# Kernel tuning notes

Measured on AMD Instinct MI355X. Metric: run time of the kernel, lower is better.

## Reference

```python
import jax, jax.numpy as jnp
import numpy as np

N = 100000
E = 1600000
IN_FEATS = 128
N_HIDDEN = 128
N_CLASSES = 40
EPS = 1e-5


def _gconv(x, W, b, src, dst, n):
    # DGL GraphConv with norm='both': D_out^{-1/2} A D_in^{-1/2} X W (+ b), degrees clamped to >=1
    ones = jnp.ones(src.shape[0], x.dtype)
    out_deg = jnp.clip(jax.ops.segment_sum(ones, src, num_segments=n), 1.0)
    in_deg = jnp.clip(jax.ops.segment_sum(ones, dst, num_segments=n), 1.0)
    h = x * (out_deg ** -0.5)[:, None]
    agg = jax.ops.segment_sum(h[src], dst, num_segments=n)  # SpMM
    agg = agg * (in_deg ** -0.5)[:, None]
    out = agg @ W
    return out + b if b is not None else out


def setup_inputs() -> dict:
    key = jax.random.key(0)
    ks = jax.random.split(key, 16)
    s = lambda fan: 1.0 / np.sqrt(fan)
    feat = jax.random.normal(ks[0], (N, IN_FEATS), dtype=jnp.float32)
    src = jax.random.randint(ks[1], (E,), 0, N, dtype=jnp.int32)
    dst = jax.random.randint(ks[2], (E,), 0, N, dtype=jnp.int32)
    # backward convs: in_feats -> in_hidden (128->128 all layers); bias only at last layer
    Wb = jax.random.uniform(ks[3], (3, IN_FEATS, N_HIDDEN), jnp.float32, -s(IN_FEATS), s(IN_FEATS))
    bb2 = jax.random.uniform(ks[4], (N_HIDDEN,), jnp.float32, -s(IN_FEATS), s(IN_FEATS))
    # forward convs: layers 0,1 are 128->128, layer 2 is 128->40 with bias
    Wh01 = jax.random.uniform(ks[5], (2, N_HIDDEN, N_HIDDEN), jnp.float32, -s(N_HIDDEN), s(N_HIDDEN))
    W2 = jax.random.uniform(ks[6], (N_HIDDEN, N_CLASSES), jnp.float32, -s(N_HIDDEN), s(N_HIDDEN))
    b2 = jax.random.uniform(ks[7], (N_CLASSES,), jnp.float32, -s(N_HIDDEN), s(N_HIDDEN))
    # linear branch (use_linear=True), no bias
    Wl01 = jax.random.uniform(ks[8], (2, N_HIDDEN, N_HIDDEN), jnp.float32, -s(N_HIDDEN), s(N_HIDDEN))
    Wl2 = jax.random.uniform(ks[9], (N_HIDDEN, N_CLASSES), jnp.float32, -s(N_HIDDEN), s(N_HIDDEN))
    gamma = jnp.ones((2, N_HIDDEN), jnp.float32)
    beta = jnp.zeros((2, N_HIDDEN), jnp.float32)
    return {"feat": feat, "Wb": Wb, "bb2": bb2, "Wh01": Wh01, "W2": W2, "b2": b2,
            "Wl01": Wl01, "Wl2": Wl2, "gamma": gamma, "beta": beta, "src": src, "dst": dst}


def reference(feat, Wb, bb2, Wh01, W2, b2, Wl01, Wl2, gamma, beta, src, dst):
    n = feat.shape[0]
    h = feat  # dropout is identity in eval
    for i in range(3):
        last = i == 2
        # backward GraphConv on reversed graph, always applied to raw input features
        hb = _gconv(feat, Wb[i], bb2 if last else None, dst, src, n)
        h = jnp.maximum(h, hb)
        W = W2 if last else Wh01[i]
        Wl = Wl2 if last else Wl01[i]
        h = _gconv(h, W, b2 if last else None, src, dst, n) + h @ Wl
        if not last:
            mu = jnp.mean(h, axis=0)
            var = jnp.var(h, axis=0)
            h = (h - mu) * jax.lax.rsqrt(var + EPS) * gamma[i] + beta[i]
            h = jax.nn.relu(h)
    return h
```

## Files before the change

### kernel.cpp

```cpp
#include <hip/hip_runtime.h>

#define NN 100000
#define NE 1600000
#define KF 128
#define NCLS 40
#define EPSV 1e-5f
#define SCAN_NB ((NN + 1023) / 1024)

typedef short bf16x8 __attribute__((ext_vector_type(8)));
typedef float f32x4 __attribute__((ext_vector_type(4)));
typedef unsigned short ushort;
typedef unsigned int uint;
typedef ushort ush8 __attribute__((ext_vector_type(8)));

static __device__ __forceinline__ int imax1(int x) { return x > 0 ? x : 1; }

static __device__ __forceinline__ ushort f2b(float f) {
  uint u = __builtin_bit_cast(uint, f);
  u += 0x7fffu + ((u >> 16) & 1u);
  return (ushort)(u >> 16);
}
static __device__ __forceinline__ float b2f(uint bits16) {
  return __builtin_bit_cast(float, bits16 << 16);
}

__global__ void k_deg(const int* __restrict__ src, const int* __restrict__ dst,
                      int* __restrict__ deg_out, int* __restrict__ deg_in,
                      uint* __restrict__ rank) {
  int e = blockIdx.x * blockDim.x + threadIdx.x;
  if (e < NE) {
    int rs = atomicAdd(&deg_out[src[e]], 1);
    int rd = atomicAdd(&deg_in[dst[e]], 1);
    rank[e] = ((uint)rd << 16) | (uint)rs;
  }
}

__global__ __launch_bounds__(256) void k_scan_part(const int* __restrict__ deg_in,
                                                   const int* __restrict__ deg_out,
                                                   int* __restrict__ bsum) {
  int arr = (int)(blockIdx.x >= SCAN_NB);
  const int* deg = arr ? deg_out : deg_in;
  int b = blockIdx.x - arr * SCAN_NB;
  int base = b * 1024 + threadIdx.x * 4;
  int4 v = {0, 0, 0, 0};
  if (base < NN) v = *(const int4*)(deg + base);
  int s = v.x + v.y + v.z + v.w;
  __shared__ int sm[256];
  sm[threadIdx.x] = s;
  __syncthreads();
  for (int d = 128; d > 0; d >>= 1) {
    if (threadIdx.x < d) sm[threadIdx.x] += sm[threadIdx.x + d];
    __syncthreads();
  }
  if (threadIdx.x == 0) bsum[blockIdx.x] = sm[0];
}

__global__ __launch_bounds__(256) void k_scan_mid(int* __restrict__ bsum) {
  __shared__ int sm[2][128];
  int t = threadIdx.x & 127;
  int seg = threadIdx.x >> 7;
  int v = (t < SCAN_NB) ? bsum[seg * SCAN_NB + t] : 0;
  sm[seg][t] = v;
  __syncthreads();
  for (int d = 1; d < 128; d <<= 1) {
    int x = (t >= d) ? sm[seg][t - d] : 0;
    __syncthreads();
    sm[seg][t] += x;
    __syncthreads();
  }
  if (t < SCAN_NB) bsum[seg * SCAN_NB + t] = sm[seg][t] - v;
}

__global__ __launch_bounds__(256) void k_scan_out(const int* __restrict__ deg_in,
                                                  const int* __restrict__ deg_out,
                                                  const int* __restrict__ bsum,
                                                  int* __restrict__ ptr_f, int* __restrict__ ptr_r) {
  int arr = (int)(blockIdx.x >= SCAN_NB);
  const int* deg = arr ? deg_out : deg_in;
  int* ptr = arr ? ptr_r : ptr_f;
  int b = blockIdx.x - arr * SCAN_NB;
  int base = b * 1024 + threadIdx.x * 4;
  int4 v = {0, 0, 0, 0};
  if (base < NN) v = *(const int4*)(deg + base);
  int s = v.x + v.y + v.z + v.w;
  __shared__ int sm[256];
  sm[threadIdx.x] = s;
  __syncthreads();
  for (int d = 1; d < 256; d <<= 1) {
    int x = (threadIdx.x >= d) ? sm[threadIdx.x - d] : 0;
    __syncthreads();
    sm[threadIdx.x] += x;
    __syncthreads();
  }
  int off = bsum[blockIdx.x] + sm[threadIdx.x] - s;
  if (base < NN) {
    int4 o;
    o.x = off;
    o.y = off + v.x;
    o.z = off + v.x + v.y;
    o.w = off + v.x + v.y + v.z;
    *(int4*)(ptr + base) = o;
  }
  if (blockIdx.x == 0 && threadIdx.x == 0) { ptr_f[NN] = NE; ptr_r[NN] = NE; }
}

__global__ void k_rsq(const int* __restrict__ deg_out, const int* __restrict__ deg_in,
                      float* __restrict__ ro, float* __restrict__ ri) {
  int i = blockIdx.x * blockDim.x + threadIdx.x;
  if (i < NN) {
    ro[i] = rsqrtf((float)imax1(deg_out[i]));
    ri[i] = rsqrtf((float)imax1(deg_in[i]));
  }
}

__global__ void k_scatter(const int* __restrict__ src, const int* __restrict__ dst,
                          const int* __restrict__ ptr_f, const int* __restrict__ ptr_r,
                          const uint* __restrict__ rank,
                          int* __restrict__ idx_f, int* __restrict__ idx_r) {
  int e = blockIdx.x * blockDim.x + threadIdx.x;
  if (e < NE) {
    int s = src[e], d = dst[e];
    uint rk = rank[e];
    idx_f[ptr_f[d] + (int)(rk >> 16)] = s;
    idx_r[ptr_r[s] + (int)(rk & 0xffffu)] = d;
  }
}

__global__ __launch_bounds__(256) void k_convF(const float* __restrict__ in, const float* __restrict__ ri,
                       ushort* __restrict__ out) {
  int t = blockIdx.x * blockDim.x + threadIdx.x;
  int i = t * 8;
  float w = ri[t >> 4];
  float4 a = *(const float4*)(in + i);
  float4 b = *(const float4*)(in + i + 4);
  ush8 o;
  o[0] = f2b(a.x * w); o[1] = f2b(a.y * w); o[2] = f2b(a.z * w); o[3] = f2b(a.w * w);
  o[4] = f2b(b.x * w); o[5] = f2b(b.y * w); o[6] = f2b(b.z * w); o[7] = f2b(b.w * w);
  *(ush8*)(out + i) = o;
}

#define WT_W2 (7 * 16384)
#define WT_L2 (WT_W2 + NCLS * KF)
__global__ __launch_bounds__(256) void k_convW(const float* __restrict__ Wb, const float* __restrict__ Wh01,
                       const float* __restrict__ Wl01, const float* __restrict__ W2,
                       const float* __restrict__ Wl2, ushort* __restrict__ wt) {
  int i = blockIdx.x * blockDim.x + threadIdx.x;
  float v;
  if (i < WT_W2) {
    int m = i >> 14, r = (i >> 7) & 127, k = i & 127;
    const float* srcm = (m < 3) ? (Wb + m * 16384)
                      : (m < 5) ? (Wh01 + (m - 3) * 16384)
                                : (Wl01 + (m - 5) * 16384);
    v = srcm[k * KF + r];
  } else {
    int j = i - WT_W2;
    int m2 = j / (NCLS * KF);
    int t = j - m2 * (NCLS * KF);
    int n = t >> 7, k = t & 127;
    v = (m2 ? Wl2 : W2)[k * NCLS + n];
  }
  wt[i] = f2b(v);
}

__global__ __launch_bounds__(256) void k_spmm_b(const ushort* __restrict__ in,
                      const int* __restrict__ ptr, const int* __restrict__ idx,
                      const float* __restrict__ wout, ushort* __restrict__ out) {
  int wid = (blockIdx.x * blockDim.x + threadIdx.x) >> 6;
  int lane = threadIdx.x & 63;
  if (wid >= NN) return;
  int beg = ptr[wid], end = ptr[wid + 1];
  int strm = lane >> 4;
  int c8 = (lane & 15) * 8;
  float s[8];
#pragma unroll
  for (int j = 0; j < 8; ++j) s[j] = 0.f;
  int p = beg + strm;
  for (; p + 4 < end; p += 8) {
    int u0 = idx[p], u1 = idx[p + 4];
    uint4 v0 = *(const uint4*)(in + (size_t)u0 * KF + c8);
    uint4 v1 = *(const uint4*)(in + (size_t)u1 * KF + c8);
    s[0] += b2f(v0.x & 0xffffu) + b2f(v1.x & 0xffffu);
    s[1] += b2f(v0.x >> 16)     + b2f(v1.x >> 16);
    s[2] += b2f(v0.y & 0xffffu) + b2f(v1.y & 0xffffu);
    s[3] += b2f(v0.y >> 16)     + b2f(v1.y >> 16);
    s[4] += b2f(v0.z & 0xffffu) + b2f(v1.z & 0xffffu);
    s[5] += b2f(v0.z >> 16)     + b2f(v1.z >> 16);
    s[6] += b2f(v0.w & 0xffffu) + b2f(v1.w & 0xffffu);
    s[7] += b2f(v0.w >> 16)     + b2f(v1.w >> 16);
  }
  if (p < end) {
    int u0 = idx[p];
    uint4 v0 = *(const uint4*)(in + (size_t)u0 * KF + c8);
    s[0] += b2f(v0.x & 0xffffu);
    s[1] += b2f(v0.x >> 16);
    s[2] += b2f(v0.y & 0xffffu);
    s[3] += b2f(v0.y >> 16);
    s[4] += b2f(v0.z & 0xffffu);
    s[5] += b2f(v0.z >> 16);
    s[6] += b2f(v0.w & 0xffffu);
    s[7] += b2f(v0.w >> 16);
  }
#pragma unroll
  for (int j = 0; j < 8; ++j) {
    s[j] += __shfl_xor(s[j], 16);
    s[j] += __shfl_xor(s[j], 32);
  }
  if (lane < 16) {
    float w = wout[wid];
    ush8 o;
#pragma unroll
    for (int j = 0; j < 8; ++j) o[j] = f2b(s[j] * w);
    *(ush8*)(out + (size_t)wid * KF + c8) = o;
  }
}

template <int NCT, bool DUAL, int EPI, bool HASB, bool NORMP>
__global__ __launch_bounds__(256) void k_gemm(
    const ushort* __restrict__ A1, const ushort* __restrict__ Wt1,
    const ushort* __restrict__ A2, const ushort* __restrict__ Wt2,
    const float* __restrict__ bias, const void* __restrict__ hprev,
    const float* __restrict__ ab, const float* __restrict__ rosc,
    float* __restrict__ outf, ushort* __restrict__ outb, ushort* __restrict__ outs,
    float* __restrict__ stat) {
  int lane = threadIdx.x & 63;
  int w = threadIdx.x >> 6;
  int r0 = blockIdx.x * 64 + w * 16;
  int arow = r0 + (lane & 15);
  if (arow > NN - 1) arow = NN - 1;
  int k0 = (lane >> 4) * 8;

  bf16x8 a1[4], a2[4];
#pragma unroll
  for (int ks = 0; ks < 4; ++ks) {
    a1[ks] = *(const bf16x8*)(A1 + (size_t)arow * KF + ks * 32 + k0);
    if (DUAL) a2[ks] = *(const bf16x8*)(A2 + (size_t)arow * KF + ks * 32 + k0);
  }
  f32x4 acc[NCT];
#pragma unroll
  for (int ct = 0; ct < NCT; ++ct) acc[ct] = (f32x4){0.f, 0.f, 0.f, 0.f};

#pragma unroll
  for (int ks = 0; ks < 4; ++ks) {
#pragma unroll
    for (int ct = 0; ct < NCT; ++ct) {
      int ncol = ct * 16 + (lane & 15);
      if (EPI == 2 && ncol > NCLS - 1) ncol = NCLS - 1;
      bf16x8 b1 = *(const bf16x8*)(Wt1 + (size_t)ncol * KF + ks * 32 + k0);
      acc[ct] = __builtin_amdgcn_mfma_f32_16x16x32_bf16(a1[ks], b1, acc[ct], 0, 0, 0);
      if (DUAL) {
        bf16x8 b2 = *(const bf16x8*)(Wt2 + (size_t)ncol * KF + ks * 32 + k0);
        acc[ct] = __builtin_amdgcn_mfma_f32_16x16x32_bf16(a2[ks], b2, acc[ct], 0, 0, 0);
      }
    }
  }

  int rbase = r0 + (lane >> 4) * 4;
  if constexpr (EPI == 0) {
    float rsc[4];
#pragma unroll
    for (int j = 0; j < 4; ++j) rsc[j] = rosc[min(rbase + j, NN - 1)];
#pragma unroll
    for (int ct = 0; ct < NCT; ++ct) {
      int col = ct * 16 + (lane & 15);
#pragma unroll
      for (int j = 0; j < 4; ++j) {
        int rr = rbase + j;
        if (rr >= NN) continue;
        float v = acc[ct][j];
        if (HASB) v += bias[col];
        float p;
        if (NORMP)
          p = fmaxf(0.f, b2f((uint)((const ushort*)hprev)[(size_t)rr * KF + col]) * ab[col] + ab[KF + col]);
        else
          p = ((const float*)hprev)[(size_t)rr * KF + col];
        float hv = fmaxf(p, v);
        outb[(size_t)rr * KF + col] = f2b(hv);
        outs[(size_t)rr * KF + col] = f2b(hv * rsc[j]);
      }
    }
  } else if constexpr (EPI == 1) {
    __shared__ float smS[4][128];
    __shared__ float smQ[4][128];
    float colS[NCT], colQ[NCT];
#pragma unroll
    for (int ct = 0; ct < NCT; ++ct) { colS[ct] = 0.f; colQ[ct] = 0.f; }
#pragma unroll
    for (int ct = 0; ct < NCT; ++ct) {
      int col = ct * 16 + (lane & 15);
#pragma unroll
      for (int j = 0; j < 4; ++j) {
        int rr = rbase + j;
        if (rr >= NN) continue;
        float v = acc[ct][j];
        outb[(size_t)rr * KF + col] = f2b(v);
        colS[ct] += v;
        colQ[ct] += v * v;
      }
    }
#pragma unroll
    for (int ct = 0; ct < NCT; ++ct) {
      colS[ct] += __shfl_xor(colS[ct], 16);
      colS[ct] += __shfl_xor(colS[ct], 32);
      colQ[ct] += __shfl_xor(colQ[ct], 16);
      colQ[ct] += __shfl_xor(colQ[ct], 32);
    }
    if (lane < 16) {
#pragma unroll
      for (int ct = 0; ct < NCT; ++ct) {
        smS[w][ct * 16 + lane] = colS[ct];
        smQ[w][ct * 16 + lane] = colQ[ct];
      }
    }
    __syncthreads();
    int tid = threadIdx.x;
    if (tid < 128)
      atomicAdd(&stat[tid], smS[0][tid] + smS[1][tid] + smS[2][tid] + smS[3][tid]);
    else
      atomicAdd(&stat[tid], smQ[0][tid - 128] + smQ[1][tid - 128] + smQ[2][tid - 128] + smQ[3][tid - 128]);
  } else {
#pragma unroll
    for (int ct = 0; ct < NCT; ++ct) {
      int col = ct * 16 + (lane & 15);
#pragma unroll
      for (int j = 0; j < 4; ++j) {
        int rr = rbase + j;
        if (rr >= NN) continue;
        if (col < NCLS) outf[(size_t)rr * NCLS + col] = acc[ct][j] + bias[col];
      }
    }
  }
}

__global__ void k_stats_fin(const float* __restrict__ stat, const float* __restrict__ gamma,
                            const float* __restrict__ beta, float* __restrict__ ab) {
  int c = threadIdx.x;
  float s = stat[c], q = stat[128 + c];
  float mu = s / (float)NN;
  float var = q / (float)NN - mu * mu;
  float rs = rsqrtf(var + EPSV);
  float a = gamma[c] * rs;
  ab[c] = a;
  ab[KF + c] = beta[c] - mu * a;
}

extern "C" void kernel_launch(void* const* d_in, const int* in_sizes, int n_in,
                              void* d_out, int out_size, void* d_ws, size_t ws_size,
                              hipStream_t stream) {
  const float* feat  = (const float*)d_in[0];
  const float* Wb    = (const float*)d_in[1];
  const float* bb2   = (const float*)d_in[2];
  const float* Wh01  = (const float*)d_in[3];
  const float* W2    = (const float*)d_in[4];
  const float* b2    = (const float*)d_in[5];
  const float* Wl01  = (const float*)d_in[6];
  const float* Wl2   = (const float*)d_in[7];
  const float* gamma = (const float*)d_in[8];
  const float* beta  = (const float*)d_in[9];
  const int* src = (const int*)d_in[10];
  const int* dst = (const int*)d_in[11];
  float* out = (float*)d_out;

  char* ws = (char*)d_ws;
  size_t off = 0;
  auto alloc = [&](size_t b) { size_t o = off; off += (b + 255) & ~(size_t)255; return o; };
  size_t z0 = alloc((size_t)(2 * NN + 2 * 256) * 4);
  int* deg_out = (int*)(ws + z0);
  int* deg_in = deg_out + NN;
  float* stat = (float*)(deg_in + NN);
  int* ptr_f = (int*)(ws + alloc((size_t)(NN + 1) * 4));
  int* ptr_r = (int*)(ws + alloc((size_t)(NN + 1) * 4));
  int* idx_f = (int*)(ws + alloc((size_t)NE * 4));
  int* idx_r = (int*)(ws + alloc((size_t)NE * 4));
  uint* rank = (uint*)(ws + alloc((size_t)NE * 4));
  float* ro = (float*)(ws + alloc((size_t)NN * 4));
  float* ri = (float*)(ws + alloc((size_t)NN * 4));
  int* bsum = (int*)(ws + alloc((size_t)2 * SCAN_NB * 4));
  ushort* featb = (ushort*)(ws + alloc((size_t)NN * KF * 2));
  ushort* aggb  = (ushort*)(ws + alloc((size_t)NN * KF * 2));
  ushort* hmaxb = (ushort*)(ws + alloc((size_t)NN * KF * 2));
  ushort* hmaxs = (ushort*)(ws + alloc((size_t)NN * KF * 2));
  float* ab = (float*)(ws + alloc((size_t)256 * 4));
  ushort* wt = (ushort*)(ws + alloc((size_t)(WT_L2 + NCLS * KF) * 2));
  ushort* t1b = featb;
  (void)ws_size;

  hipMemsetAsync(ws + z0, 0, (size_t)(2 * NN + 2 * 256) * 4, stream);
  int eb = (NE + 255) / 256;
  k_deg<<<eb, 256, 0, stream>>>(src, dst, deg_out, deg_in, rank);
  k_scan_part<<<2 * SCAN_NB, 256, 0, stream>>>(deg_in, deg_out, bsum);
  k_scan_mid<<<1, 256, 0, stream>>>(bsum);
  k_scan_out<<<2 * SCAN_NB, 256, 0, stream>>>(deg_in, deg_out, bsum, ptr_f, ptr_r);
  k_rsq<<<(NN + 255) / 256, 256, 0, stream>>>(deg_out, deg_in, ro, ri);
  k_scatter<<<eb, 256, 0, stream>>>(src, dst, ptr_f, ptr_r, rank, idx_f, idx_r);
  k_convW<<<(WT_L2 + NCLS * KF + 255) / 256, 256, 0, stream>>>(Wb, Wh01, Wl01, W2, Wl2, wt);
  k_convF<<<NN * KF / 8 / 256, 256, 0, stream>>>(feat, ri, featb);

  const ushort* wtB[3] = {wt, wt + 16384, wt + 2 * 16384};
  const ushort* wtH[2] = {wt + 3 * 16384, wt + 4 * 16384};
  const ushort* wtL[2] = {wt + 5 * 16384, wt + 6 * 16384};
  const ushort* wtW2 = wt + WT_W2;
  const ushort* wtL2 = wt + WT_L2;

  int sb = (NN * 64 + 255) / 256;
  k_spmm_b<<<sb, 256, 0, stream>>>(featb, ptr_r, idx_r, ro, aggb);

  int mb = (NN + 63) / 64;
  k_gemm<8, false, 0, false, false><<<mb, 256, 0, stream>>>(
      aggb, wtB[0], nullptr, nullptr, nullptr, feat, nullptr, ro, nullptr, hmaxb, hmaxs, nullptr);
  k_spmm_b<<<sb, 256, 0, stream>>>(hmaxs, ptr_f, idx_f, ri, t1b);
  k_gemm<8, true, 1, false, false><<<mb, 256, 0, stream>>>(
      t1b, wtH[0], hmaxb, wtL[0], nullptr, nullptr, nullptr, nullptr, nullptr, hmaxb, nullptr, stat);
  k_stats_fin<<<1, 128, 0, stream>>>(stat, gamma, beta, ab);
  k_gemm<8, false, 0, false, true><<<mb, 256, 0, stream>>>(
      aggb, wtB[1], nullptr, nullptr, nullptr, hmaxb, ab, ro, nullptr, hmaxb, hmaxs, nullptr);
  k_spmm_b<<<sb, 256, 0, stream>>>(hmaxs, ptr_f, idx_f, ri, t1b);
  k_gemm<8, true, 1, false, false><<<mb, 256, 0, stream>>>(
      t1b, wtH[1], hmaxb, wtL[1], nullptr, nullptr, nullptr, nullptr, nullptr, hmaxb, nullptr, stat + 256);
  k_stats_fin<<<1, 128, 0, stream>>>(stat + 256, gamma + KF, beta + KF, ab);
  k_gemm<8, false, 0, true, true><<<mb, 256, 0, stream>>>(
      aggb, wtB[2], nullptr, nullptr, bb2, hmaxb, ab, ro, nullptr, hmaxb, hmaxs, nullptr);
  k_spmm_b<<<sb, 256, 0, stream>>>(hmaxs, ptr_f, idx_f, ri, t1b);
  k_gemm<3, true, 2, false, false><<<mb, 256, 0, stream>>>(
      t1b, wtW2, hmaxb, wtL2, b2, nullptr, nullptr, nullptr, out, nullptr, nullptr, nullptr);
}
```

Baseline: 885.3 us.

## Build CSR via two-level bucketed counting sort instead of global atomics

Replaces the global-atomic degree counting, multi-pass scan and random scatter with a bucketed counting sort. Edges are first histogrammed into 256-node buckets, then placed into bucket-contiguous pair arrays with block-local atomics, and finally each bucket builds its degrees, row pointers and column indices in shared memory. The goal is to cut contended global atomics and random global writes in graph preprocessing. In exchange it adds extra passes over 8-byte pair buffers and uses more workspace. A bucket holding more than 6144 edges falls back to reading its pairs again from global memory.

```diff
diff --git a/kernel.cpp b/kernel.cpp
--- a/kernel.cpp
+++ b/kernel.cpp
@@ -5,7 +5,11 @@
 #define KF 128
 #define NCLS 40
 #define EPSV 1e-5f
-#define SCAN_NB ((NN + 1023) / 1024)
+#define NBUK 391
+#define TBUK 782
+#define EPB 4096
+#define P1B ((NE + EPB - 1) / EPB)
+#define CAP 6144
 
 typedef short bf16x8 __attribute__((ext_vector_type(8)));
 typedef float f32x4 __attribute__((ext_vector_type(4)));
@@ -24,84 +28,127 @@
   return __builtin_bit_cast(float, bits16 << 16);
 }
 
-__global__ void k_deg(const int* __restrict__ src, const int* __restrict__ dst,
-                      int* __restrict__ deg_out, int* __restrict__ deg_in,
-                      uint* __restrict__ rank) {
-  int e = blockIdx.x * blockDim.x + threadIdx.x;
-  if (e < NE) {
-    int rs = atomicAdd(&deg_out[src[e]], 1);
-    int rd = atomicAdd(&deg_in[dst[e]], 1);
-    rank[e] = ((uint)rd << 16) | (uint)rs;
-  }
-}
-
-__global__ __launch_bounds__(256) void k_scan_part(const int* __restrict__ deg_in,
-                                                   const int* __restrict__ deg_out,
-                                                   int* __restrict__ bsum) {
-  int arr = (int)(blockIdx.x >= SCAN_NB);
-  const int* deg = arr ? deg_out : deg_in;
-  int b = blockIdx.x - arr * SCAN_NB;
-  int base = b * 1024 + threadIdx.x * 4;
-  int4 v = {0, 0, 0, 0};
-  if (base < NN) v = *(const int4*)(deg + base);
-  int s = v.x + v.y + v.z + v.w;
-  __shared__ int sm[256];
-  sm[threadIdx.x] = s;
-  __syncthreads();
-  for (int d = 128; d > 0; d >>= 1) {
-    if (threadIdx.x < d) sm[threadIdx.x] += sm[threadIdx.x + d];
+
+__global__ __launch_bounds__(256) void kb_hist(const int* __restrict__ src, const int* __restrict__ dst,
+                                               int* __restrict__ gcount) {
+  __shared__ int hist[TBUK];
+  for (int t = threadIdx.x; t < TBUK; t += 256) hist[t] = 0;
+  __syncthreads();
+  int base = blockIdx.x * EPB + threadIdx.x;
+#pragma unroll
+  for (int i = 0; i < 16; ++i) {
+    int e = base + i * 256;
+    if (e < NE) {
+      atomicAdd(&hist[dst[e] >> 8], 1);
+      atomicAdd(&hist[NBUK + (src[e] >> 8)], 1);
+    }
+  }
+  __syncthreads();
+  for (int t = threadIdx.x; t < TBUK; t += 256)
+    if (hist[t]) atomicAdd(&gcount[t], hist[t]);
+}
+
+__global__ __launch_bounds__(1024) void kb_scan(const int* __restrict__ gcount,
+                                                int* __restrict__ gbase, int* __restrict__ gcur) {
+  __shared__ int sm[1024];
+  int t = threadIdx.x;
+  int v = (t < TBUK) ? gcount[t] : 0;
+  sm[t] = v;
+  __syncthreads();
+  for (int d = 1; d < 1024; d <<= 1) {
+    int x = (t >= d) ? sm[t - d] : 0;
     __syncthreads();
-  }
-  if (threadIdx.x == 0) bsum[blockIdx.x] = sm[0];
-}
-
-__global__ __launch_bounds__(256) void k_scan_mid(int* __restrict__ bsum) {
-  __shared__ int sm[2][128];
-  int t = threadIdx.x & 127;
-  int seg = threadIdx.x >> 7;
-  int v = (t < SCAN_NB) ? bsum[seg * SCAN_NB + t] : 0;
-  sm[seg][t] = v;
-  __syncthreads();
-  for (int d = 1; d < 128; d <<= 1) {
-    int x = (t >= d) ? sm[seg][t - d] : 0;
+    sm[t] += x;
     __syncthreads();
-    sm[seg][t] += x;
+  }
+  int excl = sm[t] - v;
+  if (t <= TBUK) gbase[t] = excl;
+  if (t < TBUK) gcur[t] = excl;
+}
+
+__global__ __launch_bounds__(256) void kb_place(const int* __restrict__ src, const int* __restrict__ dst,
+                                                int* __restrict__ gcur,
+                                                uint2* __restrict__ pairs_f, uint2* __restrict__ pairs_r) {
+  __shared__ uint2 stage[EPB];
+  __shared__ int hist[TBUK];
+  __shared__ int sbase[TBUK];
+  for (int t = threadIdx.x; t < TBUK; t += 256) hist[t] = 0;
+  __syncthreads();
+  int base = blockIdx.x * EPB;
+  int nloc = min(EPB, NE - base);
+  for (int i = threadIdx.x; i < nloc; i += 256) {
+    int e = base + i;
+    uint2 p;
+    p.x = (uint)src[e];
+    p.y = (uint)dst[e];
+    stage[i] = p;
+    atomicAdd(&hist[p.y >> 8], 1);
+    atomicAdd(&hist[NBUK + (p.x >> 8)], 1);
+  }
+  __syncthreads();
+  for (int t = threadIdx.x; t < TBUK; t += 256)
+    sbase[t] = hist[t] ? atomicAdd(&gcur[t], hist[t]) : 0;
+  __syncthreads();
+  for (int i = threadIdx.x; i < nloc; i += 256) {
+    uint2 p = stage[i];
+    int pf = atomicAdd(&sbase[p.y >> 8], 1);
+    int pr = atomicAdd(&sbase[NBUK + (p.x >> 8)], 1);
+    pairs_f[pf] = make_uint2(p.y, p.x);
+    pairs_r[pr - NE] = make_uint2(p.x, p.y);
+  }
+}
+
+__global__ __launch_bounds__(256) void kb_build(const uint2* __restrict__ pairs_f,
+                                                const uint2* __restrict__ pairs_r,
+                                                const int* __restrict__ gbase,
+                                                int* __restrict__ idx_f, int* __restrict__ idx_r,
+                                                int* __restrict__ ptr_f, int* __restrict__ ptr_r,
+                                                int* __restrict__ deg_in, int* __restrict__ deg_out) {
+  __shared__ uint2 stage[CAP];
+  __shared__ int deg[256];
+  __shared__ int ss[256];
+  __shared__ int cur[256];
+  int b = blockIdx.x;
+  int rev = (int)(b >= NBUK);
+  int k = b - rev * NBUK;
+  const uint2* pairs = rev ? pairs_r : pairs_f;
+  int* idx = rev ? idx_r : idx_f;
+  int* ptr = rev ? ptr_r : ptr_f;
+  int* degA = rev ? deg_out : deg_in;
+  int gb = gbase[b];
+  int cnt = gbase[b + 1] - gb;
+  int base = gb - rev * NE;
+  int lo = k << 8;
+  int t = threadIdx.x;
+  deg[t] = 0;
+  __syncthreads();
+  for (int i = t; i < cnt; i += 256) {
+    uint2 p = pairs[base + i];
+    if (i < CAP) stage[i] = p;
+    atomicAdd(&deg[(int)p.x - lo], 1);
+  }
+  __syncthreads();
+  int dv = deg[t];
+  if (lo + t < NN) degA[lo + t] = dv;
+  ss[t] = dv;
+  __syncthreads();
+  for (int d = 1; d < 256; d <<= 1) {
+    int x = (t >= d) ? ss[t - d] : 0;
     __syncthreads();
-  }
-  if (t < SCAN_NB) bsum[seg * SCAN_NB + t] = sm[seg][t] - v;
-}
-
-__global__ __launch_bounds__(256) void k_scan_out(const int* __restrict__ deg_in,
-                                                  const int* __restrict__ deg_out,
-                                                  const int* __restrict__ bsum,
-                                                  int* __restrict__ ptr_f, int* __restrict__ ptr_r) {
-  int arr = (int)(blockIdx.x >= SCAN_NB);
-  const int* deg = arr ? deg_out : deg_in;
-  int* ptr = arr ? ptr_r : ptr_f;
-  int b = blockIdx.x - arr * SCAN_NB;
-  int base = b * 1024 + threadIdx.x * 4;
-  int4 v = {0, 0, 0, 0};
-  if (base < NN) v = *(const int4*)(deg + base);
-  int s = v.x + v.y + v.z + v.w;
-  __shared__ int sm[256];
-  sm[threadIdx.x] = s;
-  __syncthreads();
-  for (int d = 1; d < 256; d <<= 1) {
-    int x = (threadIdx.x >= d) ? sm[threadIdx.x - d] : 0;
+    ss[t] += x;
     __syncthreads();
-    sm[threadIdx.x] += x;
-    __syncthreads();
-  }
-  int off = bsum[blockIdx.x] + sm[threadIdx.x] - s;
-  if (base < NN) {
-    int4 o;
-    o.x = off;
-    o.y = off + v.x;
-    o.z = off + v.x + v.y;
-    o.w = off + v.x + v.y + v.z;
-    *(int4*)(ptr + base) = o;
-  }
-  if (blockIdx.x == 0 && threadIdx.x == 0) { ptr_f[NN] = NE; ptr_r[NN] = NE; }
+  }
+  int ex = ss[t] - dv;
+  if (lo + t < NN) ptr[lo + t] = base + ex;
+  cur[t] = ex;
+  if (b == NBUK - 1 && t == 0) ptr_f[NN] = NE;
+  if (b == TBUK - 1 && t == 0) ptr_r[NN] = NE;
+  __syncthreads();
+  for (int i = t; i < cnt; i += 256) {
+    uint2 p = (i < CAP) ? stage[i] : pairs[base + i];
+    int pos = atomicAdd(&cur[(int)p.x - lo], 1);
+    idx[base + pos] = (int)p.y;
+  }
 }
 
 __global__ void k_rsq(const int* __restrict__ deg_out, const int* __restrict__ deg_in,
@@ -110,19 +157,6 @@
   if (i < NN) {
     ro[i] = rsqrtf((float)imax1(deg_out[i]));
     ri[i] = rsqrtf((float)imax1(deg_in[i]));
-  }
-}
-
-__global__ void k_scatter(const int* __restrict__ src, const int* __restrict__ dst,
-                          const int* __restrict__ ptr_f, const int* __restrict__ ptr_r,
-                          const uint* __restrict__ rank,
-                          int* __restrict__ idx_f, int* __restrict__ idx_r) {
-  int e = blockIdx.x * blockDim.x + threadIdx.x;
-  if (e < NE) {
-    int s = src[e], d = dst[e];
-    uint rk = rank[e];
-    idx_f[ptr_f[d] + (int)(rk >> 16)] = s;
-    idx_r[ptr_r[s] + (int)(rk & 0xffffu)] = d;
   }
 }
 
@@ -363,18 +397,21 @@
   char* ws = (char*)d_ws;
   size_t off = 0;
   auto alloc = [&](size_t b) { size_t o = off; off += (b + 255) & ~(size_t)255; return o; };
-  size_t z0 = alloc((size_t)(2 * NN + 2 * 256) * 4);
-  int* deg_out = (int*)(ws + z0);
-  int* deg_in = deg_out + NN;
-  float* stat = (float*)(deg_in + NN);
+  size_t z0 = alloc((size_t)(TBUK + 512) * 4);
+  int* gcount = (int*)(ws + z0);
+  float* stat = (float*)(gcount + TBUK);
+  int* gbase = (int*)(ws + alloc((size_t)(TBUK + 1) * 4));
+  int* gcur  = (int*)(ws + alloc((size_t)TBUK * 4));
+  int* deg_out = (int*)(ws + alloc((size_t)NN * 4));
+  int* deg_in  = (int*)(ws + alloc((size_t)NN * 4));
   int* ptr_f = (int*)(ws + alloc((size_t)(NN + 1) * 4));
   int* ptr_r = (int*)(ws + alloc((size_t)(NN + 1) * 4));
   int* idx_f = (int*)(ws + alloc((size_t)NE * 4));
   int* idx_r = (int*)(ws + alloc((size_t)NE * 4));
-  uint* rank = (uint*)(ws + alloc((size_t)NE * 4));
+  uint2* pairs_f = (uint2*)(ws + alloc((size_t)NE * 8));
+  uint2* pairs_r = (uint2*)(ws + alloc((size_t)NE * 8));
   float* ro = (float*)(ws + alloc((size_t)NN * 4));
   float* ri = (float*)(ws + alloc((size_t)NN * 4));
-  int* bsum = (int*)(ws + alloc((size_t)2 * SCAN_NB * 4));
   ushort* featb = (ushort*)(ws + alloc((size_t)NN * KF * 2));
   ushort* aggb  = (ushort*)(ws + alloc((size_t)NN * KF * 2));
   ushort* hmaxb = (ushort*)(ws + alloc((size_t)NN * KF * 2));
@@ -384,14 +421,13 @@
   ushort* t1b = featb;
   (void)ws_size;
 
-  hipMemsetAsync(ws + z0, 0, (size_t)(2 * NN + 2 * 256) * 4, stream);
-  int eb = (NE + 255) / 256;
-  k_deg<<<eb, 256, 0, stream>>>(src, dst, deg_out, deg_in, rank);
-  k_scan_part<<<2 * SCAN_NB, 256, 0, stream>>>(deg_in, deg_out, bsum);
-  k_scan_mid<<<1, 256, 0, stream>>>(bsum);
-  k_scan_out<<<2 * SCAN_NB, 256, 0, stream>>>(deg_in, deg_out, bsum, ptr_f, ptr_r);
+  hipMemsetAsync(ws + z0, 0, (size_t)(TBUK + 512) * 4, stream);
+  kb_hist<<<P1B, 256, 0, stream>>>(src, dst, gcount);
+  kb_scan<<<1, 1024, 0, stream>>>(gcount, gbase, gcur);
+  kb_place<<<P1B, 256, 0, stream>>>(src, dst, gcur, pairs_f, pairs_r);
+  kb_build<<<TBUK, 256, 0, stream>>>(pairs_f, pairs_r, gbase, idx_f, idx_r,
+                                     ptr_f, ptr_r, deg_in, deg_out);
   k_rsq<<<(NN + 255) / 256, 256, 0, stream>>>(deg_out, deg_in, ro, ri);
-  k_scatter<<<eb, 256, 0, stream>>>(src, dst, ptr_f, ptr_r, rank, idx_f, idx_r);
   k_convW<<<(WT_L2 + NCLS * KF + 255) / 256, 256, 0, stream>>>(Wb, Wh01, Wl01, W2, Wl2, wt);
   k_convF<<<NN * KF / 8 / 256, 256, 0, stream>>>(feat, ri, featb);
 
```

New measurement: 821.7 us. 1.08x faster.
